# Kernel optimization log

Hardware: AMD Instinct MI355X
Metric: run time of the kernel (lower is better)

## Reference

```python
import jax, jax.numpy as jnp
from jax import lax
import numpy as np

NODE_COUNT = 4096
BATCH = 128
THRESHOLD = 1.0
DISSIPATION = 0.1
SPARSITY = 0.9
MAX_ITERS = 100


def setup_inputs() -> dict:
    key = jax.random.key(0)
    k_in, k_conn, k_mask, k_w, k_b = jax.random.split(key, 5)
    input_data = jax.random.normal(k_in, (BATCH, NODE_COUNT), dtype=jnp.float32)
    conn = jax.random.normal(k_conn, (NODE_COUNT, NODE_COUNT), dtype=jnp.float32)
    mask = (jax.random.uniform(k_mask, (NODE_COUNT, NODE_COUNT)) > SPARSITY).astype(jnp.float32)
    conn = conn * mask
    conn = conn / (jnp.abs(conn).sum(axis=1, keepdims=True) + 1e-6)
    # input_proj: Linear(node_count, node_count), torch default init scale
    bound = 1.0 / np.sqrt(NODE_COUNT)
    W = jax.random.uniform(k_w, (NODE_COUNT, NODE_COUNT), minval=-bound, maxval=bound, dtype=jnp.float32)
    b = jax.random.uniform(k_b, (NODE_COUNT,), minval=-bound, maxval=bound, dtype=jnp.float32)
    return {"input_data": input_data, "W": W, "b": b, "connections": conn}


def _avalanche(state, connections):
    """Batched avalanche scan with per-sample sticky early-exit (torch break)."""
    B = state.shape[0]
    done0 = jnp.zeros((B,), dtype=bool)
    total0 = jnp.zeros((B,), dtype=state.dtype)

    def step(carry, _):
        state, done, total = carry
        active = (state > THRESHOLD).astype(state.dtype)          # [B, N]
        n_active = active.sum(axis=1)                              # [B]
        new_done = done | (n_active == 0)                          # break condition
        total = total + jnp.where(new_done, 0.0, n_active)
        # propagated = connections @ active  (per sample)
        prop = jnp.einsum('ij,bj->bi', connections, active)        # [B, N]
        new_state = (state * (1.0 - DISSIPATION) + prop * (1.0 - active)) * (1.0 - active)
        state = jnp.where(new_done[:, None], state, new_state)
        return (state, new_done, total), None

    (state, done, total), _ = lax.scan(step, (state, done0, total0), None, length=MAX_ITERS)
    return state, total


def reference(input_data, W, b, connections):
    projected = input_data @ W.T + b                               # [B, N]
    output, sizes = _avalanche(projected, connections)
    max_size = sizes.max()
    return output, max_size
```

## Files before the change

### kernel.cpp

```cpp
#include <hip/hip_runtime.h>

#define N_NODES 4096
#define BATCH 128
#define SPLITK 8
#define GBN 32
#define GBK 64
#define KCHUNK (N_NODES / SPLITK)
#define NSTEP (KCHUNK / GBK)
#define GEMM_BLOCKS ((N_NODES / GBN) * SPLITK)
#define TRANS_BLOCKS (64 * 64)

typedef _Float16 f16x4 __attribute__((ext_vector_type(4)));
typedef _Float16 f16x8 __attribute__((ext_vector_type(8)));
typedef float f32x4 __attribute__((ext_vector_type(4)));
typedef unsigned int u32x4 __attribute__((ext_vector_type(4)));

__device__ __forceinline__ void dma16(const void* g, void* l) {
#if defined(__has_builtin) && __has_builtin(__builtin_amdgcn_global_load_lds)
  __builtin_amdgcn_global_load_lds((const __attribute__((address_space(1))) void*)g,
                                   (__attribute__((address_space(3))) void*)l, 16, 0, 0);
#else
  *(u32x4*)l = *(const u32x4*)g;
#endif
}

#if defined(__has_builtin)
#if __has_builtin(__builtin_amdgcn_cvt_f32_fp8) && __has_builtin(__builtin_amdgcn_cvt_pk_fp8_f32)
#define CONN_FP8 1
#endif
#endif
#ifndef CONN_FP8
#define CONN_FP8 0
#endif

#if CONN_FP8
#define CONN_ELEM_BYTES 1
#define CONN_SCALE (1.0f / 256.0f)
#else
#define CONN_ELEM_BYTES 2
#define CONN_SCALE 1.0f
#endif

__device__ __forceinline__ void conn_store4(void* out, size_t off, float4 v) {
#if CONN_FP8
  unsigned int p = __builtin_amdgcn_cvt_pk_fp8_f32(v.x * 256.0f, v.y * 256.0f, 0, false);
  p = (unsigned int)__builtin_amdgcn_cvt_pk_fp8_f32(v.z * 256.0f, v.w * 256.0f, (int)p, true);
  *(unsigned int*)((unsigned char*)out + off) = p;
#else
  const unsigned int ux = __float_as_uint(v.x), uy = __float_as_uint(v.y);
  const unsigned int uz = __float_as_uint(v.z), uw = __float_as_uint(v.w);
  ushort4 u;
  u.x = (unsigned short)((ux + 0x7FFFu + ((ux >> 16) & 1u)) >> 16);
  u.y = (unsigned short)((uy + 0x7FFFu + ((uy >> 16) & 1u)) >> 16);
  u.z = (unsigned short)((uz + 0x7FFFu + ((uz >> 16) & 1u)) >> 16);
  u.w = (unsigned short)((uw + 0x7FFFu + ((uw >> 16) & 1u)) >> 16);
  *(ushort4*)((unsigned short*)out + off) = u;
#endif
}

__device__ __forceinline__ float4 conn_load4(const void* cT, int j, int t) {
#if CONN_FP8
  const unsigned int c = *(const unsigned int*)((const unsigned char*)cT + ((size_t)j << 12) + t * 4);
  return make_float4(__builtin_amdgcn_cvt_f32_fp8(c, 0), __builtin_amdgcn_cvt_f32_fp8(c, 1),
                     __builtin_amdgcn_cvt_f32_fp8(c, 2), __builtin_amdgcn_cvt_f32_fp8(c, 3));
#else
  const ushort4 c = *(const ushort4*)((const unsigned short*)cT + ((size_t)j << 12) + t * 4);
  return make_float4(__uint_as_float((unsigned int)c.x << 16),
                     __uint_as_float((unsigned int)c.y << 16),
                     __uint_as_float((unsigned int)c.z << 16),
                     __uint_as_float((unsigned int)c.w << 16));
#endif
}

__global__ __launch_bounds__(256) void asplit_kernel(const float* __restrict__ in,
                                                     _Float16* __restrict__ Ah,
                                                     _Float16* __restrict__ Al,
                                                     unsigned int* __restrict__ maxslot) {
  if (blockIdx.x == 0 && threadIdx.x == 0) *maxslot = 0u;
  const size_t idx = ((size_t)blockIdx.x * 256 + threadIdx.x) * 4;
  const float4 v = *(const float4*)(in + idx);
  f16x4 hi, lo;
  const float x0 = v.x * 256.f, x1 = v.y * 256.f, x2 = v.z * 256.f, x3 = v.w * 256.f;
  hi[0] = (_Float16)x0; lo[0] = (_Float16)(x0 - (float)hi[0]);
  hi[1] = (_Float16)x1; lo[1] = (_Float16)(x1 - (float)hi[1]);
  hi[2] = (_Float16)x2; lo[2] = (_Float16)(x2 - (float)hi[2]);
  hi[3] = (_Float16)x3; lo[3] = (_Float16)(x3 - (float)hi[3]);
  *(f16x4*)(Ah + idx) = hi;
  *(f16x4*)(Al + idx) = lo;
}

struct GemmSmem {
  alignas(16) _Float16 Ah[128 * GBK];
  alignas(16) _Float16 Al[128 * GBK];
  alignas(16) float B[GBN * GBK];
};
struct TransSmem { float tile[64][65]; };
union PrepSmem { GemmSmem g; TransSmem t; };

__global__ __launch_bounds__(256, 4) void fused_prep_kernel(
    const _Float16* __restrict__ Ah, const _Float16* __restrict__ Al,
    const float* __restrict__ W, const float* __restrict__ conn,
    float* __restrict__ P, void* __restrict__ connT) {
  __shared__ PrepSmem sm;
  const int tid = threadIdx.x;
  const int bid = blockIdx.x;

  if (bid < GEMM_BLOCKS) {
    const int wave = tid >> 6, lane = tid & 63;
    const int wm = wave >> 1, wn = wave & 1;
    const int g = lane >> 4, lrow = lane & 15;
    const int n0 = (bid & 127) * GBN;
    const int kb = (bid >> 7) * KCHUNK;

    const char* AsrcBase = (const char*)((wave >> 1) ? Al : Ah);
    _Float16* AldsBase = (wave >> 1) ? sm.g.Al : sm.g.Ah;
    const int ac0 = (wave & 1) * 8;
    const int arow_l = lane >> 3;
    const int ainrow = (((lane & 7) << 4) ^ ((lane >> 3) << 4));
    const int brow_l = lane >> 4;
    const int binrow0 = (lane & 15) << 4;

    auto issue = [&](int t) {
      const size_t kbyteA = (size_t)(kb + t * GBK) * 2;
      const size_t kbyteB = (size_t)(kb + t * GBK) * 4;
#pragma unroll
      for (int i = 0; i < 8; ++i) {
        const int c = ac0 + i;
        const int row = 8 * c + arow_l;
        dma16(AsrcBase + (size_t)row * (N_NODES * 2) + kbyteA + ainrow,
              (char*)AldsBase + c * 1024 + lane * 16);
      }
#pragma unroll
      for (int i = 0; i < 2; ++i) {
        const int c = wave * 2 + i;
        const int row = 4 * c + brow_l;
        dma16((const char*)W + (size_t)(n0 + row) * (N_NODES * 4) + kbyteB +
                  (binrow0 ^ ((row & 7) << 4)),
              (char*)sm.g.B + c * 1024 + lane * 16);
      }
    };

    f32x4 acc[4] = {};
    issue(0);
    for (int t = 0; t < NSTEP; ++t) {
      __syncthreads();
#pragma unroll
      for (int kk = 0; kk < 2; ++kk) {
        const int br = wn * 16 + lrow;
        const char* bbase = (const char*)sm.g.B + br * 256;
        const int bm = (br & 7) << 4;
        const int cb = (kk * 32 + g * 8) * 4;
        const f32x4 b0 = *(const f32x4*)(bbase + ((cb) ^ bm));
        const f32x4 b1 = *(const f32x4*)(bbase + ((cb + 16) ^ bm));
        f16x8 bh, bl;
#pragma unroll
        for (int j = 0; j < 4; ++j) {
          const float x = b0[j] * 64.f;
          const _Float16 h = (_Float16)x;
          bh[j] = h; bl[j] = (_Float16)(x - (float)h);
          const float y = b1[j] * 64.f;
          const _Float16 h2 = (_Float16)y;
          bh[4 + j] = h2; bl[4 + j] = (_Float16)(y - (float)h2);
        }
#pragma unroll
        for (int fm = 0; fm < 4; ++fm) {
          const int ar = wm * 64 + fm * 16 + lrow;
          const int am = (ar & 7) << 4;
          const int ca = (kk * 32 + g * 8) * 2;
          const f16x8 ah = *(const f16x8*)((const char*)sm.g.Ah + ar * 128 + (ca ^ am));
          const f16x8 al = *(const f16x8*)((const char*)sm.g.Al + ar * 128 + (ca ^ am));
          acc[fm] = __builtin_amdgcn_mfma_f32_16x16x32_f16(ah, bh, acc[fm], 0, 0, 0);
          acc[fm] = __builtin_amdgcn_mfma_f32_16x16x32_f16(ah, bl, acc[fm], 0, 0, 0);
          acc[fm] = __builtin_amdgcn_mfma_f32_16x16x32_f16(al, bh, acc[fm], 0, 0, 0);
        }
      }
      __syncthreads();
      if (t + 1 < NSTEP) issue(t + 1);
    }

    constexpr float INV = 1.0f / 16384.0f;
    float* Pb = P + (size_t)(bid >> 7) * BATCH * N_NODES;
    const int n = n0 + wn * 16 + lrow;
#pragma unroll
    for (int fm = 0; fm < 4; ++fm)
#pragma unroll
      for (int reg = 0; reg < 4; ++reg) {
        const int m = wm * 64 + fm * 16 + g * 4 + reg;
        Pb[(size_t)m * N_NODES + n] = acc[fm][reg] * INV;
      }
  } else {
    const int idx = bid - GEMM_BLOCKS;
    const int bx = idx & 63, by = idx >> 6;
    const int tx = tid & 15, ty = tid >> 4;
#pragma unroll
    for (int r = 0; r < 4; ++r) {
      const float4 v =
          *(const float4*)(conn + (size_t)(by * 64 + ty + 16 * r) * N_NODES + bx * 64 + tx * 4);
      sm.t.tile[ty + 16 * r][tx * 4 + 0] = v.x;
      sm.t.tile[ty + 16 * r][tx * 4 + 1] = v.y;
      sm.t.tile[ty + 16 * r][tx * 4 + 2] = v.z;
      sm.t.tile[ty + 16 * r][tx * 4 + 3] = v.w;
    }
    __syncthreads();
#pragma unroll
    for (int r = 0; r < 4; ++r) {
      const int orow = ty + 16 * r;
      float4 v;
      v.x = sm.t.tile[tx * 4 + 0][orow];
      v.y = sm.t.tile[tx * 4 + 1][orow];
      v.z = sm.t.tile[tx * 4 + 2][orow];
      v.w = sm.t.tile[tx * 4 + 3][orow];
      conn_store4(connT, (size_t)(bx * 64 + orow) * N_NODES + by * 64 + tx * 4, v);
    }
  }
}

__global__ __launch_bounds__(256) void proj_gemm_valu(const float* __restrict__ A,
                                                      const float* __restrict__ W,
                                                      float* __restrict__ P,
                                                      unsigned int* __restrict__ maxslot) {
  if (blockIdx.x == 0 && threadIdx.x == 0) *maxslot = 0u;
  __shared__ float As[16][132];
  __shared__ float Bs[16][68];
  const int tid = threadIdx.x;
  const int n0 = blockIdx.x * 64;
  const int tx = tid & 15, ty = tid >> 4;
  const int arow = tid >> 1, acol = (tid & 1) * 8;
  const int brow = tid >> 2, bcol = (tid & 3) * 4;
  float acc[2][4][4] = {};
  const float* Aptr = A + (size_t)arow * N_NODES + acol;
  const float* Wptr = W + (size_t)(n0 + brow) * N_NODES + bcol;
  for (int k0 = 0; k0 < N_NODES; k0 += 16) {
    const float4 a0 = *(const float4*)(Aptr + k0);
    const float4 a1 = *(const float4*)(Aptr + k0 + 4);
    const float4 bv = *(const float4*)(Wptr + k0);
    __syncthreads();
    As[acol + 0][arow] = a0.x; As[acol + 1][arow] = a0.y;
    As[acol + 2][arow] = a0.z; As[acol + 3][arow] = a0.w;
    As[acol + 4][arow] = a1.x; As[acol + 5][arow] = a1.y;
    As[acol + 6][arow] = a1.z; As[acol + 7][arow] = a1.w;
    Bs[bcol + 0][brow] = bv.x; Bs[bcol + 1][brow] = bv.y;
    Bs[bcol + 2][brow] = bv.z; Bs[bcol + 3][brow] = bv.w;
    __syncthreads();
#pragma unroll
    for (int kk = 0; kk < 16; ++kk) {
      const float4 av0 = *(const float4*)&As[kk][ty * 4];
      const float4 av1 = *(const float4*)&As[kk][64 + ty * 4];
      const float4 bv4 = *(const float4*)&Bs[kk][tx * 4];
      const float am[8] = {av0.x, av0.y, av0.z, av0.w, av1.x, av1.y, av1.z, av1.w};
      const float bn[4] = {bv4.x, bv4.y, bv4.z, bv4.w};
#pragma unroll
      for (int i2 = 0; i2 < 2; ++i2)
#pragma unroll
        for (int i = 0; i < 4; ++i)
#pragma unroll
          for (int j = 0; j < 4; ++j)
            acc[i2][i][j] += am[i2 * 4 + i] * bn[j];
    }
  }
#pragma unroll
  for (int i2 = 0; i2 < 2; ++i2)
#pragma unroll
    for (int i = 0; i < 4; ++i) {
      const int m = i2 * 64 + ty * 4 + i;
      *(float4*)(P + (size_t)m * N_NODES + n0 + tx * 4) =
          make_float4(acc[i2][i][0], acc[i2][i][1], acc[i2][i][2], acc[i2][i][3]);
    }
}

__global__ __launch_bounds__(256) void bias_inplace_kernel(float* __restrict__ P,
                                                           const float* __restrict__ bias) {
  const size_t base = ((size_t)blockIdx.x * 256 + threadIdx.x) * 4;
  const int n = (int)(base & (N_NODES - 1));
  float4 s = *(const float4*)(P + base);
  const float4 bv = *(const float4*)(bias + n);
  s.x += bv.x; s.y += bv.y; s.z += bv.z; s.w += bv.w;
  *(float4*)(P + base) = s;
}

template <int MODE, int NSPLIT>
__global__ __launch_bounds__(1024) void avalanche_kernel(const float* __restrict__ Pin,
                                                         const float* __restrict__ bias,
                                                         const void* __restrict__ connv,
                                                         float* __restrict__ out,
                                                         unsigned int* __restrict__ maxslot) {
  const int b = blockIdx.x;
  const int t = threadIdx.x;
  __shared__ unsigned long long mask[64];
  __shared__ int wincl[64];
  __shared__ int list[N_NODES];

  float4 s;
  if (MODE == 1) {
    const float4 bv = *(const float4*)(bias + t * 4);
    s = bv;
#pragma unroll
    for (int sp = 0; sp < NSPLIT; ++sp) {
      const float4 v = *(const float4*)(Pin + (size_t)sp * BATCH * N_NODES +
                                        (size_t)b * N_NODES + t * 4);
      s.x += v.x; s.y += v.y; s.z += v.z; s.w += v.w;
    }
  } else {
    s = *(const float4*)(Pin + (size_t)b * N_NODES + t * 4);
  }

  float total = 0.0f;

  for (int it = 0; it < 100; ++it) {
    const float v0 = s.x, v1 = s.y, v2 = s.z, v3 = s.w;
    unsigned int bits = 0;
    if (v0 > 1.0f) bits |= 1u;
    if (v1 > 1.0f) bits |= 2u;
    if (v2 > 1.0f) bits |= 4u;
    if (v3 > 1.0f) bits |= 8u;

    __syncthreads();
    if (t < 64) mask[t] = 0ULL;
    __syncthreads();
    if (bits) atomicOr(&mask[t >> 4], (unsigned long long)bits << ((t & 15) * 4));
    __syncthreads();

    if (t < 64) {
      int incl = __popcll(mask[t]);
#pragma unroll
      for (int d = 1; d < 64; d <<= 1) {
        const int y = __shfl_up(incl, d);
        if (t >= d) incl += y;
      }
      wincl[t] = incl;
    }
    __syncthreads();
    const int n = wincl[63];
    if (n == 0) break;
    total += (float)n;

    if (t < 64) {
      unsigned long long m = mask[t];
      int o = wincl[t] - __popcll(m);
      while (m) {
        list[o++] = (t << 6) + __builtin_ctzll(m);
        m &= m - 1;
      }
    }
    __syncthreads();

    float4 a0 = make_float4(0.f, 0.f, 0.f, 0.f), a1 = a0, a2 = a0, a3 = a0;
    if (MODE == 1) {
      int idx = 0;
      for (; idx + 8 <= n; idx += 8) {
        const float4 c0 = conn_load4(connv, list[idx + 0], t);
        const float4 c1 = conn_load4(connv, list[idx + 1], t);
        const float4 c2 = conn_load4(connv, list[idx + 2], t);
        const float4 c3 = conn_load4(connv, list[idx + 3], t);
        const float4 c4 = conn_load4(connv, list[idx + 4], t);
        const float4 c5 = conn_load4(connv, list[idx + 5], t);
        const float4 c6 = conn_load4(connv, list[idx + 6], t);
        const float4 c7 = conn_load4(connv, list[idx + 7], t);
        a0.x += c0.x; a0.y += c0.y; a0.z += c0.z; a0.w += c0.w;
        a1.x += c1.x; a1.y += c1.y; a1.z += c1.z; a1.w += c1.w;
        a2.x += c2.x; a2.y += c2.y; a2.z += c2.z; a2.w += c2.w;
        a3.x += c3.x; a3.y += c3.y; a3.z += c3.z; a3.w += c3.w;
        a0.x += c4.x; a0.y += c4.y; a0.z += c4.z; a0.w += c4.w;
        a1.x += c5.x; a1.y += c5.y; a1.z += c5.z; a1.w += c5.w;
        a2.x += c6.x; a2.y += c6.y; a2.z += c6.z; a2.w += c6.w;
        a3.x += c7.x; a3.y += c7.y; a3.z += c7.z; a3.w += c7.w;
      }
      for (; idx < n; ++idx) {
        const float4 c = conn_load4(connv, list[idx], t);
        a0.x += c.x; a0.y += c.y; a0.z += c.z; a0.w += c.w;
      }
    } else {
      const float* conn = (const float*)connv;
      for (int idx = 0; idx < n; ++idx) {
        const int j = list[idx];
        a0.x += conn[(size_t)(t * 4 + 0) * N_NODES + j];
        a0.y += conn[(size_t)(t * 4 + 1) * N_NODES + j];
        a0.z += conn[(size_t)(t * 4 + 2) * N_NODES + j];
        a0.w += conn[(size_t)(t * 4 + 3) * N_NODES + j];
      }
    }
    const float sc = (MODE == 1) ? CONN_SCALE : 1.0f;
    const float4 acc = make_float4(((a0.x + a1.x) + (a2.x + a3.x)) * sc,
                                   ((a0.y + a1.y) + (a2.y + a3.y)) * sc,
                                   ((a0.z + a1.z) + (a2.z + a3.z)) * sc,
                                   ((a0.w + a1.w) + (a2.w + a3.w)) * sc);

    s.x = (v0 > 1.0f) ? 0.0f : 0.9f * v0 + acc.x;
    s.y = (v1 > 1.0f) ? 0.0f : 0.9f * v1 + acc.y;
    s.z = (v2 > 1.0f) ? 0.0f : 0.9f * v2 + acc.z;
    s.w = (v3 > 1.0f) ? 0.0f : 0.9f * v3 + acc.w;
  }

  *(float4*)(out + (size_t)b * N_NODES + t * 4) = s;
  if (t == 0) atomicMax(maxslot, __float_as_uint(total));
}

extern "C" void kernel_launch(void* const* d_in, const int* in_sizes, int n_in,
                              void* d_out, int out_size, void* d_ws, size_t ws_size,
                              hipStream_t stream) {
  const float* input = (const float*)d_in[0];
  const float* W     = (const float*)d_in[1];
  const float* bias  = (const float*)d_in[2];
  const float* conn  = (const float*)d_in[3];
  float* out = (float*)d_out;

  const size_t aplane_bytes = (size_t)BATCH * N_NODES * 2;
  const size_t connT_bytes  = (size_t)N_NODES * N_NODES * CONN_ELEM_BYTES;
  const size_t part_bytes   = (size_t)SPLITK * BATCH * N_NODES * sizeof(float);
  unsigned int* maxslot = (unsigned int*)(out + (size_t)BATCH * N_NODES);

  if (ws_size >= 2 * aplane_bytes + connT_bytes + part_bytes) {
    _Float16* Ah = (_Float16*)d_ws;
    _Float16* Al = (_Float16*)((char*)d_ws + aplane_bytes);
    void* connT  = (char*)d_ws + 2 * aplane_bytes;
    float* part  = (float*)((char*)d_ws + 2 * aplane_bytes + connT_bytes);
    asplit_kernel<<<BATCH * N_NODES / 1024, 256, 0, stream>>>(input, Ah, Al, maxslot);
    fused_prep_kernel<<<GEMM_BLOCKS + TRANS_BLOCKS, 256, 0, stream>>>(Ah, Al, W, conn, part,
                                                                      connT);
    avalanche_kernel<1, SPLITK><<<BATCH, 1024, 0, stream>>>(part, bias, connT, out, maxslot);
  } else {
    proj_gemm_valu<<<dim3(N_NODES / 64, 1), 256, 0, stream>>>(input, W, out, maxslot);
    bias_inplace_kernel<<<BATCH * N_NODES / 1024, 256, 0, stream>>>(out, bias);
    avalanche_kernel<0, 1><<<BATCH, 1024, 0, stream>>>(out, nullptr, conn, out, maxslot);
  }
}
```

Measured before the change: 67.91 us.

## Replace LDS-staged projection GEMM with per-wave direct-load MFMA tiles

Rewrites the projection GEMM in the fused prep kernel so each wave independently computes a 64x32 output tile over a K-chunk, loading fp16 A halves and fp32 W directly from global memory into registers. This drops the LDS DMA staging and the block-level barriers. Split-K also doubles from 8 to 16. It removes synchronisation and LDS traffic but loses reuse across waves, which raises global/L2 traffic and doubles the split-K partial buffers that must be reduced later.

```diff
diff --git a/kernel.cpp b/kernel.cpp
--- a/kernel.cpp
+++ b/kernel.cpp
@@ -2,27 +2,14 @@
 
 #define N_NODES 4096
 #define BATCH 128
-#define SPLITK 8
-#define GBN 32
-#define GBK 64
+#define SPLITK 16
 #define KCHUNK (N_NODES / SPLITK)
-#define NSTEP (KCHUNK / GBK)
-#define GEMM_BLOCKS ((N_NODES / GBN) * SPLITK)
+#define GEMM_BLOCKS 1024
 #define TRANS_BLOCKS (64 * 64)
 
 typedef _Float16 f16x4 __attribute__((ext_vector_type(4)));
 typedef _Float16 f16x8 __attribute__((ext_vector_type(8)));
 typedef float f32x4 __attribute__((ext_vector_type(4)));
-typedef unsigned int u32x4 __attribute__((ext_vector_type(4)));
-
-__device__ __forceinline__ void dma16(const void* g, void* l) {
-#if defined(__has_builtin) && __has_builtin(__builtin_amdgcn_global_load_lds)
-  __builtin_amdgcn_global_load_lds((const __attribute__((address_space(1))) void*)g,
-                                   (__attribute__((address_space(3))) void*)l, 16, 0, 0);
-#else
-  *(u32x4*)l = *(const u32x4*)g;
-#endif
-}
 
 #if defined(__has_builtin)
 #if __has_builtin(__builtin_amdgcn_cvt_f32_fp8) && __has_builtin(__builtin_amdgcn_cvt_pk_fp8_f32)
@@ -89,104 +76,75 @@
   *(f16x4*)(Al + idx) = lo;
 }
 
-struct GemmSmem {
-  alignas(16) _Float16 Ah[128 * GBK];
-  alignas(16) _Float16 Al[128 * GBK];
-  alignas(16) float B[GBN * GBK];
-};
 struct TransSmem { float tile[64][65]; };
-union PrepSmem { GemmSmem g; TransSmem t; };
-
-__global__ __launch_bounds__(256, 4) void fused_prep_kernel(
+
+__global__ __launch_bounds__(256) void fused_prep_kernel(
     const _Float16* __restrict__ Ah, const _Float16* __restrict__ Al,
     const float* __restrict__ W, const float* __restrict__ conn,
     float* __restrict__ P, void* __restrict__ connT) {
-  __shared__ PrepSmem sm;
+  __shared__ TransSmem sm;
   const int tid = threadIdx.x;
   const int bid = blockIdx.x;
 
   if (bid < GEMM_BLOCKS) {
     const int wave = tid >> 6, lane = tid & 63;
-    const int wm = wave >> 1, wn = wave & 1;
     const int g = lane >> 4, lrow = lane & 15;
-    const int n0 = (bid & 127) * GBN;
-    const int kb = (bid >> 7) * KCHUNK;
-
-    const char* AsrcBase = (const char*)((wave >> 1) ? Al : Ah);
-    _Float16* AldsBase = (wave >> 1) ? sm.g.Al : sm.g.Ah;
-    const int ac0 = (wave & 1) * 8;
-    const int arow_l = lane >> 3;
-    const int ainrow = (((lane & 7) << 4) ^ ((lane >> 3) << 4));
-    const int brow_l = lane >> 4;
-    const int binrow0 = (lane & 15) << 4;
-
-    auto issue = [&](int t) {
-      const size_t kbyteA = (size_t)(kb + t * GBK) * 2;
-      const size_t kbyteB = (size_t)(kb + t * GBK) * 4;
-#pragma unroll
-      for (int i = 0; i < 8; ++i) {
-        const int c = ac0 + i;
-        const int row = 8 * c + arow_l;
-        dma16(AsrcBase + (size_t)row * (N_NODES * 2) + kbyteA + ainrow,
-              (char*)AldsBase + c * 1024 + lane * 16);
-      }
-#pragma unroll
-      for (int i = 0; i < 2; ++i) {
-        const int c = wave * 2 + i;
-        const int row = 4 * c + brow_l;
-        dma16((const char*)W + (size_t)(n0 + row) * (N_NODES * 4) + kbyteB +
-                  (binrow0 ^ ((row & 7) << 4)),
-              (char*)sm.g.B + c * 1024 + lane * 16);
-      }
-    };
-
-    f32x4 acc[4] = {};
-    issue(0);
-    for (int t = 0; t < NSTEP; ++t) {
-      __syncthreads();
-#pragma unroll
-      for (int kk = 0; kk < 2; ++kk) {
-        const int br = wn * 16 + lrow;
-        const char* bbase = (const char*)sm.g.B + br * 256;
-        const int bm = (br & 7) << 4;
-        const int cb = (kk * 32 + g * 8) * 4;
-        const f32x4 b0 = *(const f32x4*)(bbase + ((cb) ^ bm));
-        const f32x4 b1 = *(const f32x4*)(bbase + ((cb + 16) ^ bm));
-        f16x8 bh, bl;
+    const int w = (bid << 2) + wave;
+    const int n0 = (w & 127) * 32;
+    const int m0 = ((w >> 7) & 1) * 64;
+    const int kb = (w >> 8) * KCHUNK;
+
+    f32x4 acc[4][2] = {};
+
+    const _Float16* Ahb = Ah + (size_t)(m0 + lrow) * N_NODES + kb + g * 8;
+    const _Float16* Alb = Al + (size_t)(m0 + lrow) * N_NODES + kb + g * 8;
+    const float* Wb0 = W + (size_t)(n0 + lrow) * N_NODES + kb + g * 8;
+    const float* Wb1 = W + (size_t)(n0 + 16 + lrow) * N_NODES + kb + g * 8;
+
+#pragma unroll
+    for (int kk = 0; kk < KCHUNK / 32; ++kk) {
+      const int ko = kk * 32;
+      f16x8 bh[2], bl[2];
+#pragma unroll
+      for (int bn = 0; bn < 2; ++bn) {
+        const float* wp = (bn ? Wb1 : Wb0) + ko;
+        const f32x4 b0 = *(const f32x4*)wp;
+        const f32x4 b1 = *(const f32x4*)(wp + 4);
 #pragma unroll
         for (int j = 0; j < 4; ++j) {
           const float x = b0[j] * 64.f;
           const _Float16 h = (_Float16)x;
-          bh[j] = h; bl[j] = (_Float16)(x - (float)h);
+          bh[bn][j] = h; bl[bn][j] = (_Float16)(x - (float)h);
           const float y = b1[j] * 64.f;
           const _Float16 h2 = (_Float16)y;
-          bh[4 + j] = h2; bl[4 + j] = (_Float16)(y - (float)h2);
+          bh[bn][4 + j] = h2; bl[bn][4 + j] = (_Float16)(y - (float)h2);
         }
-#pragma unroll
-        for (int fm = 0; fm < 4; ++fm) {
-          const int ar = wm * 64 + fm * 16 + lrow;
-          const int am = (ar & 7) << 4;
-          const int ca = (kk * 32 + g * 8) * 2;
-          const f16x8 ah = *(const f16x8*)((const char*)sm.g.Ah + ar * 128 + (ca ^ am));
-          const f16x8 al = *(const f16x8*)((const char*)sm.g.Al + ar * 128 + (ca ^ am));
-          acc[fm] = __builtin_amdgcn_mfma_f32_16x16x32_f16(ah, bh, acc[fm], 0, 0, 0);
-          acc[fm] = __builtin_amdgcn_mfma_f32_16x16x32_f16(ah, bl, acc[fm], 0, 0, 0);
-          acc[fm] = __builtin_amdgcn_mfma_f32_16x16x32_f16(al, bh, acc[fm], 0, 0, 0);
+      }
+#pragma unroll
+      for (int fm = 0; fm < 4; ++fm) {
+        const f16x8 ah = *(const f16x8*)(Ahb + (size_t)(fm * 16) * N_NODES + ko);
+        const f16x8 al = *(const f16x8*)(Alb + (size_t)(fm * 16) * N_NODES + ko);
+#pragma unroll
+        for (int bn = 0; bn < 2; ++bn) {
+          acc[fm][bn] = __builtin_amdgcn_mfma_f32_16x16x32_f16(ah, bh[bn], acc[fm][bn], 0, 0, 0);
+          acc[fm][bn] = __builtin_amdgcn_mfma_f32_16x16x32_f16(ah, bl[bn], acc[fm][bn], 0, 0, 0);
+          acc[fm][bn] = __builtin_amdgcn_mfma_f32_16x16x32_f16(al, bh[bn], acc[fm][bn], 0, 0, 0);
         }
       }
-      __syncthreads();
-      if (t + 1 < NSTEP) issue(t + 1);
     }
 
     constexpr float INV = 1.0f / 16384.0f;
-    float* Pb = P + (size_t)(bid >> 7) * BATCH * N_NODES;
-    const int n = n0 + wn * 16 + lrow;
+    float* Pb = P + (size_t)(w >> 8) * BATCH * N_NODES;
 #pragma unroll
     for (int fm = 0; fm < 4; ++fm)
 #pragma unroll
-      for (int reg = 0; reg < 4; ++reg) {
-        const int m = wm * 64 + fm * 16 + g * 4 + reg;
-        Pb[(size_t)m * N_NODES + n] = acc[fm][reg] * INV;
+      for (int bn = 0; bn < 2; ++bn) {
+        const int n = n0 + bn * 16 + lrow;
+#pragma unroll
+        for (int reg = 0; reg < 4; ++reg) {
+          const int m = m0 + fm * 16 + g * 4 + reg;
+          Pb[(size_t)m * N_NODES + n] = acc[fm][bn][reg] * INV;
+        }
       }
   } else {
     const int idx = bid - GEMM_BLOCKS;
@@ -196,20 +154,20 @@
     for (int r = 0; r < 4; ++r) {
       const float4 v =
           *(const float4*)(conn + (size_t)(by * 64 + ty + 16 * r) * N_NODES + bx * 64 + tx * 4);
-      sm.t.tile[ty + 16 * r][tx * 4 + 0] = v.x;
-      sm.t.tile[ty + 16 * r][tx * 4 + 1] = v.y;
-      sm.t.tile[ty + 16 * r][tx * 4 + 2] = v.z;
-      sm.t.tile[ty + 16 * r][tx * 4 + 3] = v.w;
+      sm.tile[ty + 16 * r][tx * 4 + 0] = v.x;
+      sm.tile[ty + 16 * r][tx * 4 + 1] = v.y;
+      sm.tile[ty + 16 * r][tx * 4 + 2] = v.z;
+      sm.tile[ty + 16 * r][tx * 4 + 3] = v.w;
     }
     __syncthreads();
 #pragma unroll
     for (int r = 0; r < 4; ++r) {
       const int orow = ty + 16 * r;
       float4 v;
-      v.x = sm.t.tile[tx * 4 + 0][orow];
-      v.y = sm.t.tile[tx * 4 + 1][orow];
-      v.z = sm.t.tile[tx * 4 + 2][orow];
-      v.w = sm.t.tile[tx * 4 + 3][orow];
+      v.x = sm.tile[tx * 4 + 0][orow];
+      v.y = sm.tile[tx * 4 + 1][orow];
+      v.z = sm.tile[tx * 4 + 2][orow];
+      v.w = sm.tile[tx * 4 + 3][orow];
       conn_store4(connT, (size_t)(bx * 64 + orow) * N_NODES + by * 64 + tx * 4, v);
     }
   }
```

Measured after the change: 94.41 us. +39.0%, slower.

## Double-buffer projection GEMM LDS tiles and make transpose per-wave tiles

Applied to the files above, without the earlier changes.

The split-K projection GEMM now keeps two LDS buffers for its A and B tiles. It prefetches two K-steps ahead and waits with explicit vmcnt counters and raw s_barrier, so the global-to-LDS DMA overlaps MFMA work instead of being serialized by __syncthreads. The connection transpose blocks now give each wave its own 64x64 tile, which removes the block barrier and cuts the transpose block count by four. Shared memory per block roughly doubles and launch bounds drop to 2 blocks per CU, which may lower occupancy.

```diff
diff --git a/kernel.cpp b/kernel.cpp
--- a/kernel.cpp
+++ b/kernel.cpp
@@ -8,7 +8,7 @@
 #define KCHUNK (N_NODES / SPLITK)
 #define NSTEP (KCHUNK / GBK)
 #define GEMM_BLOCKS ((N_NODES / GBN) * SPLITK)
-#define TRANS_BLOCKS (64 * 64)
+#define TRANS_BLOCKS 1024
 
 typedef _Float16 f16x4 __attribute__((ext_vector_type(4)));
 typedef _Float16 f16x8 __attribute__((ext_vector_type(8)));
@@ -90,45 +90,45 @@
 }
 
 struct GemmSmem {
-  alignas(16) _Float16 Ah[128 * GBK];
-  alignas(16) _Float16 Al[128 * GBK];
-  alignas(16) float B[GBN * GBK];
+  alignas(16) _Float16 Ah[2][128 * GBK];
+  alignas(16) _Float16 Al[2][128 * GBK];
+  alignas(16) float B[2][GBN * GBK];
 };
-struct TransSmem { float tile[64][65]; };
+struct TransSmem { float tile[4][64][65]; };
 union PrepSmem { GemmSmem g; TransSmem t; };
 
-__global__ __launch_bounds__(256, 4) void fused_prep_kernel(
-    const _Float16* __restrict__ Ah, const _Float16* __restrict__ Al,
+__global__ __launch_bounds__(256, 2) void fused_prep_kernel(
+    const _Float16* __restrict__ Ahp, const _Float16* __restrict__ Alp,
     const float* __restrict__ W, const float* __restrict__ conn,
     float* __restrict__ P, void* __restrict__ connT) {
   __shared__ PrepSmem sm;
   const int tid = threadIdx.x;
   const int bid = blockIdx.x;
+  const int wave = tid >> 6, lane = tid & 63;
 
   if (bid < GEMM_BLOCKS) {
-    const int wave = tid >> 6, lane = tid & 63;
     const int wm = wave >> 1, wn = wave & 1;
     const int g = lane >> 4, lrow = lane & 15;
     const int n0 = (bid & 127) * GBN;
     const int kb = (bid >> 7) * KCHUNK;
 
-    const char* AsrcBase = (const char*)((wave >> 1) ? Al : Ah);
-    _Float16* AldsBase = (wave >> 1) ? sm.g.Al : sm.g.Ah;
+    const char* AsrcBase = (const char*)((wave >> 1) ? Alp : Ahp);
     const int ac0 = (wave & 1) * 8;
     const int arow_l = lane >> 3;
     const int ainrow = (((lane & 7) << 4) ^ ((lane >> 3) << 4));
     const int brow_l = lane >> 4;
     const int binrow0 = (lane & 15) << 4;
 
-    auto issue = [&](int t) {
+    auto issue = [&](int buf, int t) {
       const size_t kbyteA = (size_t)(kb + t * GBK) * 2;
       const size_t kbyteB = (size_t)(kb + t * GBK) * 4;
+      char* AldsB = (char*)((wave >> 1) ? sm.g.Al[buf] : sm.g.Ah[buf]);
 #pragma unroll
       for (int i = 0; i < 8; ++i) {
         const int c = ac0 + i;
         const int row = 8 * c + arow_l;
         dma16(AsrcBase + (size_t)row * (N_NODES * 2) + kbyteA + ainrow,
-              (char*)AldsBase + c * 1024 + lane * 16);
+              AldsB + c * 1024 + lane * 16);
       }
 #pragma unroll
       for (int i = 0; i < 2; ++i) {
@@ -136,18 +136,27 @@
         const int row = 4 * c + brow_l;
         dma16((const char*)W + (size_t)(n0 + row) * (N_NODES * 4) + kbyteB +
                   (binrow0 ^ ((row & 7) << 4)),
-              (char*)sm.g.B + c * 1024 + lane * 16);
+              (char*)sm.g.B[buf] + c * 1024 + lane * 16);
       }
     };
 
     f32x4 acc[4] = {};
-    issue(0);
+    issue(0, 0);
+    issue(1, 1);
+
+#pragma unroll
     for (int t = 0; t < NSTEP; ++t) {
-      __syncthreads();
+      const int cur = t & 1;
+      if (t + 1 < NSTEP) asm volatile("s_waitcnt vmcnt(10)" ::: "memory");
+      else               asm volatile("s_waitcnt vmcnt(0)" ::: "memory");
+      __builtin_amdgcn_sched_barrier(0);
+      __builtin_amdgcn_s_barrier();
+      __builtin_amdgcn_sched_barrier(0);
+
 #pragma unroll
       for (int kk = 0; kk < 2; ++kk) {
         const int br = wn * 16 + lrow;
-        const char* bbase = (const char*)sm.g.B + br * 256;
+        const char* bbase = (const char*)sm.g.B[cur] + br * 256;
         const int bm = (br & 7) << 4;
         const int cb = (kk * 32 + g * 8) * 4;
         const f32x4 b0 = *(const f32x4*)(bbase + ((cb) ^ bm));
@@ -167,15 +176,18 @@
           const int ar = wm * 64 + fm * 16 + lrow;
           const int am = (ar & 7) << 4;
           const int ca = (kk * 32 + g * 8) * 2;
-          const f16x8 ah = *(const f16x8*)((const char*)sm.g.Ah + ar * 128 + (ca ^ am));
-          const f16x8 al = *(const f16x8*)((const char*)sm.g.Al + ar * 128 + (ca ^ am));
+          const f16x8 ah = *(const f16x8*)((const char*)sm.g.Ah[cur] + ar * 128 + (ca ^ am));
+          const f16x8 al = *(const f16x8*)((const char*)sm.g.Al[cur] + ar * 128 + (ca ^ am));
           acc[fm] = __builtin_amdgcn_mfma_f32_16x16x32_f16(ah, bh, acc[fm], 0, 0, 0);
           acc[fm] = __builtin_amdgcn_mfma_f32_16x16x32_f16(ah, bl, acc[fm], 0, 0, 0);
           acc[fm] = __builtin_amdgcn_mfma_f32_16x16x32_f16(al, bh, acc[fm], 0, 0, 0);
         }
       }
-      __syncthreads();
-      if (t + 1 < NSTEP) issue(t + 1);
+
+      __builtin_amdgcn_sched_barrier(0);
+      __builtin_amdgcn_s_barrier();
+      __builtin_amdgcn_sched_barrier(0);
+      if (t + 2 < NSTEP) issue(cur, t + 2);
     }
 
     constexpr float INV = 1.0f / 16384.0f;
@@ -189,28 +201,27 @@
         Pb[(size_t)m * N_NODES + n] = acc[fm][reg] * INV;
       }
   } else {
-    const int idx = bid - GEMM_BLOCKS;
-    const int bx = idx & 63, by = idx >> 6;
-    const int tx = tid & 15, ty = tid >> 4;
-#pragma unroll
-    for (int r = 0; r < 4; ++r) {
-      const float4 v =
-          *(const float4*)(conn + (size_t)(by * 64 + ty + 16 * r) * N_NODES + bx * 64 + tx * 4);
-      sm.t.tile[ty + 16 * r][tx * 4 + 0] = v.x;
-      sm.t.tile[ty + 16 * r][tx * 4 + 1] = v.y;
-      sm.t.tile[ty + 16 * r][tx * 4 + 2] = v.z;
-      sm.t.tile[ty + 16 * r][tx * 4 + 3] = v.w;
-    }
-    __syncthreads();
-#pragma unroll
-    for (int r = 0; r < 4; ++r) {
-      const int orow = ty + 16 * r;
+    const int tile_id = (bid - GEMM_BLOCKS) * 4 + wave;
+    const int bx = tile_id & 63, by = tile_id >> 6;
+    float (*T)[65] = sm.t.tile[wave];
+    const int lr = lane >> 4;
+    const int lc = lane & 15;
+#pragma unroll
+    for (int i = 0; i < 16; ++i) {
+      const int r = lr + 4 * i;
+      const float4 v = *(const float4*)(conn + (size_t)(by * 64 + r) * N_NODES + bx * 64 + lc * 4);
+      T[r][lc * 4 + 0] = v.x; T[r][lc * 4 + 1] = v.y;
+      T[r][lc * 4 + 2] = v.z; T[r][lc * 4 + 3] = v.w;
+    }
+#pragma unroll
+    for (int i = 0; i < 16; ++i) {
+      const int orow = lr + 4 * i;
       float4 v;
-      v.x = sm.t.tile[tx * 4 + 0][orow];
-      v.y = sm.t.tile[tx * 4 + 1][orow];
-      v.z = sm.t.tile[tx * 4 + 2][orow];
-      v.w = sm.t.tile[tx * 4 + 3][orow];
-      conn_store4(connT, (size_t)(bx * 64 + orow) * N_NODES + by * 64 + tx * 4, v);
+      v.x = T[lc * 4 + 0][orow];
+      v.y = T[lc * 4 + 1][orow];
+      v.z = T[lc * 4 + 2][orow];
+      v.w = T[lc * 4 + 3][orow];
+      conn_store4(connT, (size_t)(bx * 64 + orow) * N_NODES + by * 64 + lc * 4, v);
     }
   }
 }
```

Measured after the change: 70.17 us. +3.3%, slower.
